# Optimization experiments

Measured on AMD Instinct MI355X. Metric: run time of the kernel, lower is better.

Reference implementation:

```python
import jax, jax.numpy as jnp
import numpy as np
import math

B, S, D = 4, 2048, 1024

def setup_inputs() -> dict:
    key = jax.random.key(0)
    k_x, k_q, k_k, k_v = jax.random.split(key, 4)
    scale = 1.0 / math.sqrt(D)
    return {
        "x": jax.random.normal(k_x, (B, S, D), dtype=jnp.float32),
        "W_Q": jax.random.normal(k_q, (D, D), dtype=jnp.float32) * scale,
        "W_K": jax.random.normal(k_k, (D, D), dtype=jnp.float32) * scale,
        "W_V": jax.random.normal(k_v, (D, D), dtype=jnp.float32) * scale,
    }

def reference(x, W_Q, W_K, W_V):
    # nn.Linear(bias=False): y = x @ W.T
    Q = jnp.einsum('bsd,ed->bse', x, W_Q)
    K = jnp.einsum('bsd,ed->bse', x, W_K)
    V = jnp.einsum('bsd,ed->bse', x, W_V)
    scores = jnp.einsum('bqd,bkd->bqk', Q, K) / jnp.sqrt(jnp.asarray(Q.shape[-1], Q.dtype))
    weight = jax.nn.softmax(scores, axis=-1)  # [B,S,S]
    return jnp.einsum('bqk,bkd->bqd', weight, V)
```

## Files before the change

### kernel.cpp

```cpp
#include <hip/hip_runtime.h>
#include <stdint.h>

typedef __bf16 bf16;
typedef __bf16 bf16x8 __attribute__((ext_vector_type(8)));
typedef __bf16 bf16x4 __attribute__((ext_vector_type(4)));
typedef float f32x4 __attribute__((ext_vector_type(4)));

__device__ inline void gload_lds16(const void* g, void* l) {
  __builtin_amdgcn_global_load_lds(
      (__attribute__((address_space(1))) void*)g,
      (__attribute__((address_space(3))) void*)l, 16, 0, 0);
}

__device__ inline void xcd_swizzle(int& bx, int& by, int& bz) {
  const int gx = gridDim.x, gy = gridDim.y;
  int lin = blockIdx.x + gx * (blockIdx.y + gy * blockIdx.z);
  const int nwg = gx * gy * gridDim.z;
  lin = (lin & 7) * (nwg >> 3) + (lin >> 3);
  bx = lin % gx;
  const int tmp = lin / gx;
  by = tmp % gy;
  bz = tmp / gy;
}

__global__ __launch_bounds__(256) void cvt_all(
    const float* __restrict__ x, const float* __restrict__ wq,
    const float* __restrict__ wk, const float* __restrict__ wv,
    bf16* __restrict__ xb2, bf16* __restrict__ Wb2) {
  const int NX = 2097152;
  const int NW = 262144;
  int i = blockIdx.x * 256 + threadIdx.x;
  const int stride = gridDim.x * 256;
  for (int p = i; p < NX + 3 * NW; p += stride) {
    const float* src; bf16* dst; int off;
    if (p < NX) {
      src = x; off = p;
      const int row = p >> 8, c4 = p & 255;
      dst = xb2 + ((long)row << 11) + (c4 << 2);
    } else {
      int q = p - NX; const int w = q >> 18; off = q & (NW - 1);
      src = (w == 0) ? wq : ((w == 1) ? wk : wv);
      const int row = off >> 8, c4 = off & 255;
      dst = Wb2 + ((long)(w * 1024 + row) << 11) + (c4 << 2);
    }
    float4 v = ((const float4*)src)[off];
    bf16x4 o;
    o[0] = (bf16)v.x; o[1] = (bf16)v.y; o[2] = (bf16)v.z; o[3] = (bf16)v.w;
    *(bf16x4*)dst = o;
  }
}

template <int MODE>
__global__ __launch_bounds__(512, 2) void gemm8(
    const bf16* __restrict__ Ag, const bf16* __restrict__ Bg,
    void* __restrict__ Cg,
    long lda, long ldb, long ldc,
    long sA, long sB, long sC, int K, float scale)
{
  constexpr int BUFSZ = 65536;
  __shared__ alignas(16) char lds[2 * BUFSZ];
  int bx, by, bz;
  xcd_swizzle(bx, by, bz);
  const int tid = threadIdx.x;
  const int l = tid & 63;
  const int wv = tid >> 6;
  const int fr = l & 15;
  const int kch = l >> 4;
  const int m0 = by * 256;
  const int n0 = bx * 256;
  const bf16* Ab = Ag + (long)bz * sA;
  const bf16* Bb = Bg + (long)bz * sB;

  const int wm = wv >> 2;
  const int wn = wv & 3;

  const int a_rd = fr * 128 + (((wm * 4 + kch) ^ (fr & 7)) << 4);
  const int b_rd = (wn & 1) * 8192 + fr * 128 + ((((wn >> 1) * 4 + kch) ^ (fr & 7)) << 4);

  const int se = (tid & 7) ^ ((tid >> 3) & 7);
  const int s_row = (se >> 2) * 128 + (tid >> 3);
  const int s_k = (se & 3) * 8;
  const int wb16 = (tid & 448) * 16;

  const int NT = K >> 6;
  f32x4 acc[8][4] = {};

  auto stageA = [&](int tile, int kh, int buf) {
#pragma unroll
    for (int rd = 0; rd < 2; ++rd)
      gload_lds16(Ab + (long)(m0 + s_row + rd * 64) * lda + tile * 64 + kh * 32 + s_k,
                  lds + buf * BUFSZ + kh * 16384 + rd * 8192 + wb16);
  };
  auto stageB = [&](int tile, int kh, int buf) {
#pragma unroll
    for (int rd = 0; rd < 2; ++rd)
      gload_lds16(Bb + (long)(n0 + s_row + rd * 64) * ldb + tile * 64 + kh * 32 + s_k,
                  lds + buf * BUFSZ + 32768 + kh * 16384 + rd * 8192 + wb16);
  };

  stageA(0, 0, 0); stageB(0, 0, 0); stageA(0, 1, 0); stageB(0, 1, 0);
  stageA(min(1, NT - 1), 0, 1); stageB(min(1, NT - 1), 0, 1);
  asm volatile("s_waitcnt vmcnt(4)" ::: "memory");
  __builtin_amdgcn_sched_barrier(0);
  __builtin_amdgcn_s_barrier();

  for (int t = 0; t < NT; ++t) {
    const char* bufA = lds + (t & 1) * BUFSZ;
    const char* bufB = bufA + 32768;
    const int t1 = min(t + 1, NT - 1);
    const int t2 = min(t + 2, NT - 1);
    const int nb = (t & 1) ^ 1;
    const int cur = t & 1;

    bf16x8 bfg[4], af[4];
    stageA(t1, 1, nb);
#pragma unroll
    for (int n = 0; n < 4; ++n) bfg[n] = *(const bf16x8*)(bufB + n * 2048 + b_rd);
#pragma unroll
    for (int m = 0; m < 4; ++m) af[m] = *(const bf16x8*)(bufA + m * 2048 + a_rd);
    __builtin_amdgcn_s_setprio(1);
#pragma unroll
    for (int m = 0; m < 4; ++m)
#pragma unroll
      for (int n = 0; n < 4; ++n)
        acc[m][n] = __builtin_amdgcn_mfma_f32_16x16x32_bf16(af[m], bfg[n], acc[m][n], 0, 0, 0);
    __builtin_amdgcn_s_setprio(0);
    __builtin_amdgcn_s_barrier();
    stageB(t1, 1, nb);
#pragma unroll
    for (int m = 0; m < 4; ++m) af[m] = *(const bf16x8*)(bufA + 8192 + m * 2048 + a_rd);
    __builtin_amdgcn_s_setprio(1);
#pragma unroll
    for (int m = 0; m < 4; ++m)
#pragma unroll
      for (int n = 0; n < 4; ++n)
        acc[4 + m][n] = __builtin_amdgcn_mfma_f32_16x16x32_bf16(af[m], bfg[n], acc[4 + m][n], 0, 0, 0);
    __builtin_amdgcn_s_setprio(0);
    __builtin_amdgcn_s_barrier();
    stageA(t2, 0, cur);
#pragma unroll
    for (int n = 0; n < 4; ++n) bfg[n] = *(const bf16x8*)(bufB + 16384 + n * 2048 + b_rd);
#pragma unroll
    for (int m = 0; m < 4; ++m) af[m] = *(const bf16x8*)(bufA + 16384 + m * 2048 + a_rd);
    __builtin_amdgcn_s_setprio(1);
#pragma unroll
    for (int m = 0; m < 4; ++m)
#pragma unroll
      for (int n = 0; n < 4; ++n)
        acc[m][n] = __builtin_amdgcn_mfma_f32_16x16x32_bf16(af[m], bfg[n], acc[m][n], 0, 0, 0);
    __builtin_amdgcn_s_setprio(0);
    __builtin_amdgcn_s_barrier();
    stageB(t2, 0, cur);
#pragma unroll
    for (int m = 0; m < 4; ++m) af[m] = *(const bf16x8*)(bufA + 16384 + 8192 + m * 2048 + a_rd);
    __builtin_amdgcn_s_setprio(1);
#pragma unroll
    for (int m = 0; m < 4; ++m)
#pragma unroll
      for (int n = 0; n < 4; ++n)
        acc[4 + m][n] = __builtin_amdgcn_mfma_f32_16x16x32_bf16(af[m], bfg[n], acc[4 + m][n], 0, 0, 0);
    __builtin_amdgcn_s_setprio(0);
    asm volatile("s_waitcnt vmcnt(4)" ::: "memory");
    __builtin_amdgcn_sched_barrier(0);
    __builtin_amdgcn_s_barrier();
  }
  asm volatile("s_waitcnt vmcnt(0)" ::: "memory");

#pragma unroll
  for (int mf = 0; mf < 8; ++mf) {
    const int row = m0 + wm * 128 + (mf >> 2) * 64 + (mf & 3) * 16 + (l >> 4) * 4;
#pragma unroll
    for (int n = 0; n < 4; ++n) {
      const int col = n0 + wn * 64 + n * 16 + fr;
      if constexpr (MODE == 0) {
        bf16* C = (bf16*)Cg + (long)bz * sC;
#pragma unroll
        for (int r = 0; r < 4; ++r)
          C[(long)(row + r) * ldc + col] = (bf16)(acc[mf][n][r] * scale);
      } else {
        float* C = (float*)Cg + (long)bz * sC;
#pragma unroll
        for (int r = 0; r < 4; ++r)
          C[(long)(row + r) * ldc + col] = acc[mf][n][r] * scale;
      }
    }
  }
}

__global__ __launch_bounds__(512, 2) void projV(
    const bf16* __restrict__ Xg, const bf16* __restrict__ Wv,
    bf16* __restrict__ Vt)
{
  constexpr int BUFSZ = 49152;
  __shared__ alignas(16) char lds[2 * BUFSZ];
  int bx, by, bz;
  xcd_swizzle(bx, by, bz);
  const int tid = threadIdx.x;
  const int l = tid & 63;
  const int wv = tid >> 6;
  const int wm = wv >> 2;
  const int wn = wv & 3;
  const int fr = l & 15;
  const int kch = l >> 4;
  const int m0 = by * 256;
  const int n0 = bx * 128;
  const bf16* Xb = Xg + (long)bz * 4194304;

  const int a_rd = fr * 128 + (((wm * 4 + kch) ^ (fr & 7)) << 4);
  int b_off[2];
#pragma unroll
  for (int n = 0; n < 2; ++n)
    b_off[n] = 32768 + ((wn & 1) * 32 + n * 16 + fr) * 128 +
               ((((wn >> 1) * 4 + kch) ^ (fr & 7)) << 4);

  const int se = (tid & 7) ^ ((tid >> 3) & 7);
  const int s_rowA = (se >> 2) * 128 + (tid >> 3);
  const int s_rowB = (se >> 2) * 64 + (tid >> 3);
  const int s_k = (se & 3) * 8;
  const int wb16 = (tid & 448) * 16;

  const int NT = 16;
  f32x4 acc[8][2] = {};

  auto stageA = [&](int tile, int kh, int buf) {
#pragma unroll
    for (int rd = 0; rd < 2; ++rd)
      gload_lds16(Xb + (long)(m0 + s_rowA + rd * 64) * 2048 + tile * 64 + kh * 32 + s_k,
                  lds + buf * BUFSZ + kh * 16384 + rd * 8192 + wb16);
  };
  auto stageB = [&](int tile, int kh, int buf) {
    gload_lds16(Wv + (long)(n0 + s_rowB) * 2048 + tile * 64 + kh * 32 + s_k,
                lds + buf * BUFSZ + 32768 + kh * 8192 + wb16);
  };

  stageA(0, 0, 0); stageB(0, 0, 0); stageA(0, 1, 0); stageB(0, 1, 0);
  stageA(1, 0, 1); stageB(1, 0, 1);
  asm volatile("s_waitcnt vmcnt(3)" ::: "memory");
  __builtin_amdgcn_sched_barrier(0);
  __builtin_amdgcn_s_barrier();

  for (int t = 0; t < NT; ++t) {
    const char* bufA = lds + (t & 1) * BUFSZ;
    const int t1 = min(t + 1, NT - 1);
    const int t2 = min(t + 2, NT - 1);
    const int nb = (t & 1) ^ 1;
    const int cur = t & 1;

    bf16x8 bfg[2], af[4];
    stageA(t1, 1, nb);
#pragma unroll
    for (int n = 0; n < 2; ++n) bfg[n] = *(const bf16x8*)(bufA + b_off[n]);
#pragma unroll
    for (int m = 0; m < 4; ++m) af[m] = *(const bf16x8*)(bufA + m * 2048 + a_rd);
    __builtin_amdgcn_s_setprio(1);
#pragma unroll
    for (int m = 0; m < 4; ++m)
#pragma unroll
      for (int n = 0; n < 2; ++n)
        acc[m][n] = __builtin_amdgcn_mfma_f32_16x16x32_bf16(af[m], bfg[n], acc[m][n], 0, 0, 0);
    __builtin_amdgcn_s_setprio(0);
    __builtin_amdgcn_s_barrier();
    stageB(t1, 1, nb);
#pragma unroll
    for (int m = 0; m < 4; ++m) af[m] = *(const bf16x8*)(bufA + 8192 + m * 2048 + a_rd);
    __builtin_amdgcn_s_setprio(1);
#pragma unroll
    for (int m = 0; m < 4; ++m)
#pragma unroll
      for (int n = 0; n < 2; ++n)
        acc[4 + m][n] = __builtin_amdgcn_mfma_f32_16x16x32_bf16(af[m], bfg[n], acc[4 + m][n], 0, 0, 0);
    __builtin_amdgcn_s_setprio(0);
    __builtin_amdgcn_s_barrier();
    stageA(t2, 0, cur);
#pragma unroll
    for (int n = 0; n < 2; ++n) bfg[n] = *(const bf16x8*)(bufA + 8192 + b_off[n]);
#pragma unroll
    for (int m = 0; m < 4; ++m) af[m] = *(const bf16x8*)(bufA + 16384 + m * 2048 + a_rd);
    __builtin_amdgcn_s_setprio(1);
#pragma unroll
    for (int m = 0; m < 4; ++m)
#pragma unroll
      for (int n = 0; n < 2; ++n)
        acc[m][n] = __builtin_amdgcn_mfma_f32_16x16x32_bf16(af[m], bfg[n], acc[m][n], 0, 0, 0);
    __builtin_amdgcn_s_setprio(0);
    __builtin_amdgcn_s_barrier();
    stageB(t2, 0, cur);
#pragma unroll
    for (int m = 0; m < 4; ++m) af[m] = *(const bf16x8*)(bufA + 16384 + 8192 + m * 2048 + a_rd);
    __builtin_amdgcn_s_setprio(1);
#pragma unroll
    for (int m = 0; m < 4; ++m)
#pragma unroll
      for (int n = 0; n < 2; ++n)
        acc[4 + m][n] = __builtin_amdgcn_mfma_f32_16x16x32_bf16(af[m], bfg[n], acc[4 + m][n], 0, 0, 0);
    __builtin_amdgcn_s_setprio(0);
    asm volatile("s_waitcnt vmcnt(3)" ::: "memory");
    __builtin_amdgcn_sched_barrier(0);
    __builtin_amdgcn_s_barrier();
  }
  asm volatile("s_waitcnt vmcnt(0)" ::: "memory");

#pragma unroll
  for (int mf = 0; mf < 8; ++mf) {
    const int s = m0 + wm * 128 + (mf >> 2) * 64 + (mf & 3) * 16 + (l >> 4) * 4;
#pragma unroll
    for (int n = 0; n < 2; ++n) {
      const int d = n0 + wn * 32 + n * 16 + fr;
      bf16x4 pk;
#pragma unroll
      for (int r = 0; r < 4; ++r) pk[r] = (bf16)acc[mf][n][r];
      *(bf16x4*)(Vt + (long)bz * 2097152 + (long)d * 2048 + s) = pk;
    }
  }
}

__global__ __launch_bounds__(256) void softmax_k(const bf16* __restrict__ Sm,
                                                 bf16* __restrict__ P, int cols) {
  __shared__ float red[8];
  const long row = blockIdx.x;
  const bf16* sr = Sm + row * (long)cols;
  bf16* pr = P + row * (long)cols;
  const int t = threadIdx.x;
  bf16x8 v = *(const bf16x8*)(sr + t * 8);
  float e[8];
#pragma unroll
  for (int j = 0; j < 8; ++j) e[j] = (float)v[j];
  float m = e[0];
#pragma unroll
  for (int j = 1; j < 8; ++j) m = fmaxf(m, e[j]);
#pragma unroll
  for (int o = 32; o; o >>= 1) m = fmaxf(m, __shfl_xor(m, o));
  if ((t & 63) == 0) red[t >> 6] = m;
  __syncthreads();
  m = fmaxf(fmaxf(red[0], red[1]), fmaxf(red[2], red[3]));
  float s = 0.f;
#pragma unroll
  for (int j = 0; j < 8; ++j) { e[j] = __expf(e[j] - m); s += e[j]; }
#pragma unroll
  for (int o = 32; o; o >>= 1) s += __shfl_xor(s, o);
  if ((t & 63) == 0) red[4 + (t >> 6)] = s;
  __syncthreads();
  s = red[4] + red[5] + red[6] + red[7];
  const float inv = 1.0f / s;
  bf16x8 o8;
#pragma unroll
  for (int j = 0; j < 8; ++j) o8[j] = (bf16)(e[j] * inv);
  *(bf16x8*)(pr + t * 8) = o8;
}

extern "C" void kernel_launch(void* const* d_in, const int* in_sizes, int n_in,
                              void* d_out, int out_size, void* d_ws, size_t ws_size,
                              hipStream_t stream) {
  const float* x  = (const float*)d_in[0];
  const float* Wq = (const float*)d_in[1];
  const float* Wk = (const float*)d_in[2];
  const float* Wv = (const float*)d_in[3];
  float* out = (float*)d_out;

  char* ws = (char*)d_ws;
  bf16* QKbuf = (bf16*)(ws);
  bf16* P     = (bf16*)(ws);
  bf16* Vt    = (bf16*)(ws + 33554432);
  bf16* scb   = (bf16*)(ws + 50331648);
  bf16* xb2   = (bf16*)(ws + 50331648);
  bf16* Wb2   = (bf16*)(ws + 83886080);

  dim3 b256(256, 1, 1), b512(512, 1, 1);

  cvt_all<<<2048, b256, 0, stream>>>(x, Wq, Wk, Wv, xb2, Wb2);

  gemm8<0><<<dim3(8, 8, 4), b512, 0, stream>>>(
      xb2, Wb2, QKbuf, 2048, 2048, 2048,
      4194304, 0, 4194304, 1024, 1.f);

  projV<<<dim3(8, 8, 4), b512, 0, stream>>>(xb2, Wb2 + 2 * 1024 * 2048, Vt);

  gemm8<0><<<dim3(8, 8, 4), b512, 0, stream>>>(
      QKbuf, QKbuf + 1024, scb, 2048, 2048, 2048,
      4194304, 4194304, 4194304, 1024, 0.03125f);

  softmax_k<<<8192, b256, 0, stream>>>(scb, P, 2048);

  gemm8<2><<<dim3(4, 8, 4), b512, 0, stream>>>(
      P, Vt, out, 2048, 2048, 1024,
      4194304, 2097152, 2097152, 2048, 1.f);
}
```

Baseline: 181.8 us.

## Generalize projV into gemm128 for PV, add nontemporal stores and XCD-aware row mapping

The V-projection kernel becomes a templated 256x128-tile GEMM (gemm128) that also runs the final P·V product with fp32 nontemporal stores. This gives 256 workgroups instead of the 128 launched by the old 256x256 gemm8 call, so more CUs are busy. The QK projection epilogue now uses nontemporal bf16 stores. The conversion and softmax kernels remap rows so that consecutive blocks on the same XCD touch contiguous data, aiming for better L2 locality. The risks are the cost of nontemporal stores on data that the next kernel re-reads, and a smaller tile that gives less operand reuse.

```diff
diff --git a/kernel.cpp b/kernel.cpp
--- a/kernel.cpp
+++ b/kernel.cpp
@@ -10,6 +10,10 @@
   __builtin_amdgcn_global_load_lds(
       (__attribute__((address_space(1))) void*)g,
       (__attribute__((address_space(3))) void*)l, 16, 0, 0);
+}
+
+__device__ inline void nt_store_bf16(bf16* p, bf16 v) {
+  __builtin_nontemporal_store(*(const unsigned short*)&v, (unsigned short*)p);
 }
 
 __device__ inline void xcd_swizzle(int& bx, int& by, int& bz) {
@@ -27,33 +31,33 @@
     const float* __restrict__ x, const float* __restrict__ wq,
     const float* __restrict__ wk, const float* __restrict__ wv,
     bf16* __restrict__ xb2, bf16* __restrict__ Wb2) {
-  const int NX = 2097152;
-  const int NW = 262144;
-  int i = blockIdx.x * 256 + threadIdx.x;
-  const int stride = gridDim.x * 256;
-  for (int p = i; p < NX + 3 * NW; p += stride) {
-    const float* src; bf16* dst; int off;
-    if (p < NX) {
-      src = x; off = p;
-      const int row = p >> 8, c4 = p & 255;
-      dst = xb2 + ((long)row << 11) + (c4 << 2);
-    } else {
-      int q = p - NX; const int w = q >> 18; off = q & (NW - 1);
-      src = (w == 0) ? wq : ((w == 1) ? wk : wv);
-      const int row = off >> 8, c4 = off & 255;
-      dst = Wb2 + ((long)(w * 1024 + row) << 11) + (c4 << 2);
-    }
+  const int b = blockIdx.x;
+  const int t = threadIdx.x;
+  const int xcd = b & 7, j = b >> 3;
+#pragma unroll
+  for (int k = 0; k < 4; ++k) {
+    const int row = xcd * 1024 + j + 256 * k;
+    float4 v = ((const float4*)x)[(long)row * 256 + t];
+    bf16x4 o;
+    o[0] = (bf16)v.x; o[1] = (bf16)v.y; o[2] = (bf16)v.z; o[3] = (bf16)v.w;
+    *(bf16x4*)(xb2 + ((long)row << 11) + t * 4) = o;
+  }
+  for (long p = (long)b * 256 + t; p < 786432; p += 524288) {
+    const int w = (int)(p >> 18);
+    const int off = (int)(p & 262143);
+    const float* src = (w == 0) ? wq : ((w == 1) ? wk : wv);
+    const int row = off >> 8, c4 = off & 255;
     float4 v = ((const float4*)src)[off];
     bf16x4 o;
     o[0] = (bf16)v.x; o[1] = (bf16)v.y; o[2] = (bf16)v.z; o[3] = (bf16)v.w;
-    *(bf16x4*)dst = o;
+    *(bf16x4*)(Wb2 + ((long)(w * 1024 + row) << 11) + c4 * 4) = o;
   }
 }
 
 template <int MODE>
 __global__ __launch_bounds__(512, 2) void gemm8(
     const bf16* __restrict__ Ag, const bf16* __restrict__ Bg,
-    void* __restrict__ Cg,
+    bf16* __restrict__ Cg,
     long lda, long ldb, long ldc,
     long sA, long sB, long sC, int K, float scale)
 {
@@ -172,24 +176,22 @@
 #pragma unroll
     for (int n = 0; n < 4; ++n) {
       const int col = n0 + wn * 64 + n * 16 + fr;
-      if constexpr (MODE == 0) {
-        bf16* C = (bf16*)Cg + (long)bz * sC;
-#pragma unroll
-        for (int r = 0; r < 4; ++r)
-          C[(long)(row + r) * ldc + col] = (bf16)(acc[mf][n][r] * scale);
-      } else {
-        float* C = (float*)Cg + (long)bz * sC;
-#pragma unroll
-        for (int r = 0; r < 4; ++r)
-          C[(long)(row + r) * ldc + col] = acc[mf][n][r] * scale;
+      bf16* C = Cg + (long)bz * sC;
+#pragma unroll
+      for (int r = 0; r < 4; ++r) {
+        const bf16 v = (bf16)(acc[mf][n][r] * scale);
+        if constexpr (MODE == 0) C[(long)(row + r) * ldc + col] = v;
+        else                     nt_store_bf16(&C[(long)(row + r) * ldc + col], v);
       }
     }
   }
 }
 
-__global__ __launch_bounds__(512, 2) void projV(
-    const bf16* __restrict__ Xg, const bf16* __restrict__ Wv,
-    bf16* __restrict__ Vt)
+template <int MODE>
+__global__ __launch_bounds__(512, 2) void gemm128(
+    const bf16* __restrict__ Ag, const bf16* __restrict__ Bg,
+    void* __restrict__ Cg,
+    long sA, long sB, int K)
 {
   constexpr int BUFSZ = 49152;
   __shared__ alignas(16) char lds[2 * BUFSZ];
@@ -204,7 +206,8 @@
   const int kch = l >> 4;
   const int m0 = by * 256;
   const int n0 = bx * 128;
-  const bf16* Xb = Xg + (long)bz * 4194304;
+  const bf16* Ab = Ag + (long)bz * sA;
+  const bf16* Bb = Bg + (long)bz * sB;
 
   const int a_rd = fr * 128 + (((wm * 4 + kch) ^ (fr & 7)) << 4);
   int b_off[2];
@@ -219,22 +222,22 @@
   const int s_k = (se & 3) * 8;
   const int wb16 = (tid & 448) * 16;
 
-  const int NT = 16;
+  const int NT = K >> 6;
   f32x4 acc[8][2] = {};
 
   auto stageA = [&](int tile, int kh, int buf) {
 #pragma unroll
     for (int rd = 0; rd < 2; ++rd)
-      gload_lds16(Xb + (long)(m0 + s_rowA + rd * 64) * 2048 + tile * 64 + kh * 32 + s_k,
+      gload_lds16(Ab + (long)(m0 + s_rowA + rd * 64) * 2048 + tile * 64 + kh * 32 + s_k,
                   lds + buf * BUFSZ + kh * 16384 + rd * 8192 + wb16);
   };
   auto stageB = [&](int tile, int kh, int buf) {
-    gload_lds16(Wv + (long)(n0 + s_rowB) * 2048 + tile * 64 + kh * 32 + s_k,
+    gload_lds16(Bb + (long)(n0 + s_rowB) * 2048 + tile * 64 + kh * 32 + s_k,
                 lds + buf * BUFSZ + 32768 + kh * 8192 + wb16);
   };
 
   stageA(0, 0, 0); stageB(0, 0, 0); stageA(0, 1, 0); stageB(0, 1, 0);
-  stageA(1, 0, 1); stageB(1, 0, 1);
+  stageA(min(1, NT - 1), 0, 1); stageB(min(1, NT - 1), 0, 1);
   asm volatile("s_waitcnt vmcnt(3)" ::: "memory");
   __builtin_amdgcn_sched_barrier(0);
   __builtin_amdgcn_s_barrier();
@@ -302,14 +305,22 @@
 
 #pragma unroll
   for (int mf = 0; mf < 8; ++mf) {
-    const int s = m0 + wm * 128 + (mf >> 2) * 64 + (mf & 3) * 16 + (l >> 4) * 4;
+    const int row = m0 + wm * 128 + (mf >> 2) * 64 + (mf & 3) * 16 + (l >> 4) * 4;
 #pragma unroll
     for (int n = 0; n < 2; ++n) {
-      const int d = n0 + wn * 32 + n * 16 + fr;
-      bf16x4 pk;
-#pragma unroll
-      for (int r = 0; r < 4; ++r) pk[r] = (bf16)acc[mf][n][r];
-      *(bf16x4*)(Vt + (long)bz * 2097152 + (long)d * 2048 + s) = pk;
+      const int col = n0 + wn * 32 + n * 16 + fr;
+      if constexpr (MODE == 0) {
+        bf16* Vt = (bf16*)Cg;
+        bf16x4 pk;
+#pragma unroll
+        for (int r = 0; r < 4; ++r) pk[r] = (bf16)acc[mf][n][r];
+        *(bf16x4*)(Vt + (long)bz * 2097152 + (long)col * 2048 + row) = pk;
+      } else {
+        float* C = (float*)Cg + (long)bz * 2097152;
+#pragma unroll
+        for (int r = 0; r < 4; ++r)
+          __builtin_nontemporal_store(acc[mf][n][r], &C[(long)(row + r) * 1024 + col]);
+      }
     }
   }
 }
@@ -317,7 +328,8 @@
 __global__ __launch_bounds__(256) void softmax_k(const bf16* __restrict__ Sm,
                                                  bf16* __restrict__ P, int cols) {
   __shared__ float red[8];
-  const long row = blockIdx.x;
+  const int b = blockIdx.x;
+  const long row = (long)(b & 7) * 1024 + (b >> 3);
   const bf16* sr = Sm + row * (long)cols;
   bf16* pr = P + row * (long)cols;
   const int t = threadIdx.x;
@@ -369,11 +381,12 @@
 
   cvt_all<<<2048, b256, 0, stream>>>(x, Wq, Wk, Wv, xb2, Wb2);
 
-  gemm8<0><<<dim3(8, 8, 4), b512, 0, stream>>>(
+  gemm8<1><<<dim3(8, 8, 4), b512, 0, stream>>>(
       xb2, Wb2, QKbuf, 2048, 2048, 2048,
       4194304, 0, 4194304, 1024, 1.f);
 
-  projV<<<dim3(8, 8, 4), b512, 0, stream>>>(xb2, Wb2 + 2 * 1024 * 2048, Vt);
+  gemm128<0><<<dim3(8, 8, 4), b512, 0, stream>>>(
+      xb2, Wb2 + 2 * 1024 * 2048, Vt, 4194304, 0, 1024);
 
   gemm8<0><<<dim3(8, 8, 4), b512, 0, stream>>>(
       QKbuf, QKbuf + 1024, scb, 2048, 2048, 2048,
@@ -381,7 +394,6 @@
 
   softmax_k<<<8192, b256, 0, stream>>>(scb, P, 2048);
 
-  gemm8<2><<<dim3(4, 8, 4), b512, 0, stream>>>(
-      P, Vt, out, 2048, 2048, 1024,
-      4194304, 2097152, 2097152, 2048, 1.f);
-}
+  gemm128<1><<<dim3(8, 8, 4), b512, 0, stream>>>(
+      P, Vt, out, 4194304, 2097152, 2048);
+}
```

New measurement: 179.3 us. Within noise of the previous version (-1.4%).
